# Kernel optimization log

Measured on AMD Instinct MI355X. Metric: run time of the kernel, lower is better.

The kernel has to match this reference:

```python
import jax, jax.numpy as jnp
import numpy as np
from jax import lax

# ---- config (matches init_kwargs) ----
B, T, H = 4, 2048, 1024
HU = 4 * H                 # h_up = hidden*4
LAYERS, INDEX = 12, 0
K_CLAMP, K_EPS = 60.0, 1e-8
LN_EPS = 1e-5


def setup_inputs() -> dict:
    key = jax.random.key(0)
    ks = jax.random.split(key, 9)
    s = 0.02  # weight scale
    tr01 = INDEX / (LAYERS - 1)          # time_ratio_0_to_1
    tr1pz = 1.0 - INDEX / LAYERS         # time_ratio_1_to_pz
    i_h = np.arange(H, dtype=np.float64) / H
    i_hu = np.arange(HU, dtype=np.float64)
    # per-channel decay speed / first (sized to the WKV channel dim h_up)
    decay_speed = -5.0 + 8.0 * (i_hu / (HU - 1)) ** (0.7 + 1.3 * tr01)
    zigzag = ((np.arange(HU) + 1) % 3 - 1) * 0.5
    time_first = np.log(0.3) + zigzag
    f32 = lambda a: jnp.asarray(a, jnp.float32)
    return {
        "x": jax.random.normal(ks[0], (B, T, H), jnp.float32),
        "ln0_g": jnp.ones((H,), jnp.float32), "ln0_b": jnp.zeros((H,), jnp.float32),
        "pre_g": jnp.ones((H,), jnp.float32), "pre_b": jnp.zeros((H,), jnp.float32),
        "post_g": jnp.ones((H,), jnp.float32), "post_b": jnp.zeros((H,), jnp.float32),
        "tm_decay": f32(decay_speed),
        "tm_first": f32(time_first),
        "tm_mix_k": f32(i_h ** tr1pz),
        "tm_mix_v": f32(i_h ** tr1pz + 0.3 * tr01),
        "tm_mix_r": f32(i_h ** (0.5 * tr1pz)),
        "tm_Wk": jax.random.normal(ks[1], (H, HU), jnp.float32) * s,
        "tm_Wv": jax.random.normal(ks[2], (H, HU), jnp.float32) * s,
        "tm_Wr": jax.random.normal(ks[3], (H, HU), jnp.float32) * s,
        "tm_Wo": jax.random.normal(ks[4], (HU, H), jnp.float32) * s,
        "cm_mix_k": f32(i_h ** tr1pz),
        "cm_mix_r": f32(i_h ** tr1pz),
        "cm_Wk": jax.random.normal(ks[5], (H, HU), jnp.float32) * s,
        "cm_Wv": jax.random.normal(ks[6], (HU, H), jnp.float32) * s,
        "cm_Wr": jax.random.normal(ks[7], (H, H), jnp.float32) * s,
    }


def _ln(x, g, b):
    m = jnp.mean(x, -1, keepdims=True)
    v = jnp.mean((x - m) ** 2, -1, keepdims=True)
    return (x - m) / jnp.sqrt(v + LN_EPS) * g + b


def _shift(x):  # ZeroPad2d((0,0,1,-1)): xx[:, t] = x[:, t-1], xx[:, 0] = 0
    return jnp.pad(x[:, :-1], ((0, 0), (1, 0), (0, 0)))


def _wkv(k, kv, decay, first):
    # k, kv: [B, T, HU]; decay, first: [HU]
    # wkv[t] = first*kv[t] + sum_{d>=1} decay^(d-1) * kv[t-d]  (same for k)
    def step(carry, inp):
        sk, skv = carry
        kt, kvt = inp
        out = (first * kt + sk, first * kvt + skv)
        return (kt + decay * sk, kvt + decay * skv), out
    b = k.shape[0]
    init = (jnp.zeros((b, k.shape[2]), k.dtype), jnp.zeros((b, k.shape[2]), k.dtype))
    _, (wk, wkv) = lax.scan(step, init, (jnp.swapaxes(k, 0, 1), jnp.swapaxes(kv, 0, 1)))
    return jnp.swapaxes(wk, 0, 1), jnp.swapaxes(wkv, 0, 1)


def reference(x, ln0_g, ln0_b, pre_g, pre_b, post_g, post_b,
              tm_decay, tm_first, tm_mix_k, tm_mix_v, tm_mix_r,
              tm_Wk, tm_Wv, tm_Wr, tm_Wo,
              cm_mix_k, cm_mix_r, cm_Wk, cm_Wv, cm_Wr):
    if INDEX == 0:
        x = _ln(x, ln0_g, ln0_b)

    # ---- RWKV_TM (time mix / WKV) ----
    xn = _ln(x, pre_g, pre_b)
    xx = _shift(xn)
    xk = xn * tm_mix_k + xx * (1.0 - tm_mix_k)
    xv = xn * tm_mix_v + xx * (1.0 - tm_mix_v)
    xr = xn * tm_mix_r + xx * (1.0 - tm_mix_r)
    k = jnp.exp(jnp.minimum(xk @ tm_Wk, K_CLAMP))   # [B,T,HU]
    v = xv @ tm_Wv                                  # [B,T,HU]
    r = xr @ tm_Wr                                  # [B,T,HU]
    kv = k * v
    decay = jnp.exp(-jnp.exp(tm_decay))  # per-step multiplier exp(-exp(time_decay))
    first = jnp.exp(tm_first)
    wk, wkv = _wkv(k, kv, decay, first)
    rwkv = jax.nn.sigmoid(r) * (wkv / (wk + K_EPS))
    x = x + rwkv @ tm_Wo

    # ---- RWKV_CM (channel mix) ----
    xn = _ln(x, post_g, post_b)
    xx = _shift(xn)
    xk = xn * cm_mix_k + xx * (1.0 - cm_mix_k)
    xr = xn * cm_mix_r + xx * (1.0 - cm_mix_r)
    kv = jax.nn.silu(xk @ cm_Wk) @ cm_Wv            # [B,T,H]
    x = x + (jax.nn.sigmoid(xr @ cm_Wr) + kv)
    return x
```

## Files before the change

### kernel.cpp

```cpp
#include <hip/hip_runtime.h>

#define Hdim  1024
#define Tdim  2048
#define Bdim  4
#define HUdim 4096
#define Mrows (Bdim*Tdim)
#define CHUNK 2048
#define NCH   (HUdim/CHUNK)
#define NSEG  16
#define SEGL  (Tdim/NSEG)
#define SCHUNK 16

typedef __bf16 bf16;
typedef __bf16 bf16x2 __attribute__((ext_vector_type(2)));
typedef __bf16 bf16x8 __attribute__((ext_vector_type(8)));
typedef float  floatx4 __attribute__((ext_vector_type(4)));

__device__ __forceinline__ bf16 f2bf(float x) { return (bf16)x; }

__global__ __launch_bounds__(256) void wconv_all(
    const float* __restrict__ s0, const float* __restrict__ s1, const float* __restrict__ s2,
    const float* __restrict__ s3, const float* __restrict__ s4, const float* __restrict__ s5,
    const float* __restrict__ s6,
    bf16* d0, bf16* d1, bf16* d2, bf16* d3, bf16* d4, bf16* d5, bf16* d6) {
  __shared__ float tile[64][65];
  int bid = blockIdx.x;
  const float* src; bf16* dst; int K, N, local;
  if (bid < 1024)      { src = s0; dst = d0; K = Hdim;  N = HUdim; local = bid; }
  else if (bid < 2048) { src = s1; dst = d1; K = Hdim;  N = HUdim; local = bid - 1024; }
  else if (bid < 3072) { src = s2; dst = d2; K = Hdim;  N = HUdim; local = bid - 2048; }
  else if (bid < 4096) { src = s3; dst = d3; K = HUdim; N = Hdim;  local = bid - 3072; }
  else if (bid < 5120) { src = s4; dst = d4; K = Hdim;  N = HUdim; local = bid - 4096; }
  else if (bid < 6144) { src = s5; dst = d5; K = HUdim; N = Hdim;  local = bid - 5120; }
  else                 { src = s6; dst = d6; K = Hdim;  N = Hdim;  local = bid - 6144; }
  const int nt = N >> 6;
  const int n0 = (local % nt) * 64, k0 = (local / nt) * 64;
  const int tr = threadIdx.x >> 6;
  const int tc = threadIdx.x & 63;
#pragma unroll
  for (int j = 0; j < 16; j++) {
    int r = j * 4 + tr;
    tile[r][tc] = src[(size_t)(k0 + r) * N + n0 + tc];
  }
  __syncthreads();
#pragma unroll
  for (int j = 0; j < 16; j++) {
    int r = j * 4 + tr;
    dst[(size_t)(n0 + r) * K + k0 + tc] = f2bf(tile[tc][r]);
  }
}

__device__ __forceinline__ void block_reduce4(float v[4], float* sm) {
#pragma unroll
  for (int off = 32; off > 0; off >>= 1) {
#pragma unroll
    for (int i = 0; i < 4; i++) v[i] += __shfl_down(v[i], off, 64);
  }
  const int w = threadIdx.x >> 6;
  if ((threadIdx.x & 63) == 0) {
#pragma unroll
    for (int i = 0; i < 4; i++) sm[w * 4 + i] = v[i];
  }
  __syncthreads();
#pragma unroll
  for (int i = 0; i < 4; i++) v[i] = sm[i] + sm[4 + i] + sm[8 + i] + sm[12 + i];
  __syncthreads();
}

__global__ __launch_bounds__(256) void ln_mix_tm(
    const float* __restrict__ x,
    const float* __restrict__ g0, const float* __restrict__ b0,
    const float* __restrict__ g1, const float* __restrict__ b1,
    const float* __restrict__ mk, const float* __restrict__ mv, const float* __restrict__ mr,
    float* __restrict__ x0, bf16* __restrict__ xk, bf16* __restrict__ xv, bf16* __restrict__ xr) {
  __shared__ float sm[16];
  const int bid = blockIdx.x;
  const int t = bid & (Tdim - 1);
  const int tid = threadIdx.x;
  const bool havep = (t > 0);
  const float hp = havep ? 1.f : 0.f;
  const float* rowc = x + (size_t)bid * Hdim;
  const float* rowp = havep ? (rowc - Hdim) : rowc;

  float c[4], p[4];
#pragma unroll
  for (int j = 0; j < 4; j++) c[j] = rowc[tid * 4 + j];
#pragma unroll
  for (int j = 0; j < 4; j++) p[j] = rowp[tid * 4 + j] * hp;

  float red[4] = {0.f, 0.f, 0.f, 0.f};
#pragma unroll
  for (int j = 0; j < 4; j++) { red[0] += c[j]; red[1] += c[j]*c[j]; red[2] += p[j]; red[3] += p[j]*p[j]; }
  block_reduce4(red, sm);
  const float inv = 1.f / Hdim;
  float mc = red[0]*inv, vc = red[1]*inv - mc*mc;
  float mp = red[2]*inv, vp = red[3]*inv - mp*mp;
  float sc = rsqrtf(vc + 1e-5f), sp = rsqrtf(vp + 1e-5f);

  float yc[4], yp[4];
#pragma unroll
  for (int j = 0; j < 4; j++) {
    int i = tid * 4 + j;
    yc[j] = (c[j] - mc) * sc * g0[i] + b0[i];
    yp[j] = ((p[j] - mp) * sp * g0[i] + b0[i]) * hp;
    x0[(size_t)bid * Hdim + i] = yc[j];
  }

  float r2[4] = {0.f, 0.f, 0.f, 0.f};
#pragma unroll
  for (int j = 0; j < 4; j++) { r2[0] += yc[j]; r2[1] += yc[j]*yc[j]; r2[2] += yp[j]; r2[3] += yp[j]*yp[j]; }
  block_reduce4(r2, sm);
  float mc2 = r2[0]*inv, vc2 = r2[1]*inv - mc2*mc2;
  float mp2 = r2[2]*inv, vp2 = r2[3]*inv - mp2*mp2;
  float sc2 = rsqrtf(vc2 + 1e-5f), sp2 = rsqrtf(vp2 + 1e-5f);

#pragma unroll
  for (int j = 0; j < 4; j++) {
    int i = tid * 4 + j;
    float xnc = (yc[j] - mc2) * sc2 * g1[i] + b1[i];
    float xnp = ((yp[j] - mp2) * sp2 * g1[i] + b1[i]) * hp;
    size_t o = (size_t)bid * Hdim + i;
    float a;
    a = mk[i]; xk[o] = f2bf(xnc * a + xnp * (1.f - a));
    a = mv[i]; xv[o] = f2bf(xnc * a + xnp * (1.f - a));
    a = mr[i]; xr[o] = f2bf(xnc * a + xnp * (1.f - a));
  }
}

__global__ __launch_bounds__(256) void ln_mix_cm(
    const float* __restrict__ xin,
    const float* __restrict__ g, const float* __restrict__ bb,
    const float* __restrict__ mk, const float* __restrict__ mr,
    bf16* __restrict__ xk, bf16* __restrict__ xr) {
  __shared__ float sm[16];
  const int bid = blockIdx.x;
  const int t = bid & (Tdim - 1);
  const int tid = threadIdx.x;
  const bool havep = (t > 0);
  const float hp = havep ? 1.f : 0.f;
  const float* rowc = xin + (size_t)bid * Hdim;
  const float* rowp = havep ? (rowc - Hdim) : rowc;

  float c[4], p[4];
#pragma unroll
  for (int j = 0; j < 4; j++) c[j] = rowc[tid * 4 + j];
#pragma unroll
  for (int j = 0; j < 4; j++) p[j] = rowp[tid * 4 + j] * hp;

  float red[4] = {0.f, 0.f, 0.f, 0.f};
#pragma unroll
  for (int j = 0; j < 4; j++) { red[0] += c[j]; red[1] += c[j]*c[j]; red[2] += p[j]; red[3] += p[j]*p[j]; }
  block_reduce4(red, sm);
  const float inv = 1.f / Hdim;
  float mc = red[0]*inv, vc = red[1]*inv - mc*mc;
  float mp = red[2]*inv, vp = red[3]*inv - mp*mp;
  float sc = rsqrtf(vc + 1e-5f), sp = rsqrtf(vp + 1e-5f);

#pragma unroll
  for (int j = 0; j < 4; j++) {
    int i = tid * 4 + j;
    float xnc = (c[j] - mc) * sc * g[i] + bb[i];
    float xnp = ((p[j] - mp) * sp * g[i] + bb[i]) * hp;
    size_t o = (size_t)bid * Hdim + i;
    float a;
    a = mk[i]; xk[o] = f2bf(xnc * a + xnp * (1.f - a));
    a = mr[i]; xr[o] = f2bf(xnc * a + xnp * (1.f - a));
  }
}

__global__ __launch_bounds__(64) void wkv_part(
    const bf16* __restrict__ Kb, const bf16* __restrict__ Vb,
    float* __restrict__ stK, float* __restrict__ stKV,
    const float* __restrict__ tdec) {
  const int seg = blockIdx.x & (NSEG - 1);
  const int rest = blockIdx.x >> 4;
  const int b = rest >> 4, g = rest & 15;
  const int c = (g << 7) + (threadIdx.x << 1);
  const float d0 = __expf(-__expf(tdec[c]));
  const float d1 = __expf(-__expf(tdec[c + 1]));
  size_t base = ((size_t)b * Tdim + (size_t)seg * SEGL) * CHUNK + c;
  float sk0 = 0.f, skv0 = 0.f, sk1 = 0.f, skv1 = 0.f;
  for (int t0 = 0; t0 < SEGL; t0 += SCHUNK) {
    bf16x2 kk[SCHUNK], vv[SCHUNK];
#pragma unroll
    for (int j = 0; j < SCHUNK; j++) {
      size_t idx = base + (size_t)(t0 + j) * CHUNK;
      kk[j] = *(const bf16x2*)(Kb + idx);
      vv[j] = *(const bf16x2*)(Vb + idx);
    }
#pragma unroll
    for (int j = 0; j < SCHUNK; j++) {
      float k0 = (float)kk[j][0], k1 = (float)kk[j][1];
      float v0 = (float)vv[j][0], v1 = (float)vv[j][1];
      sk0  = fmaf(d0, sk0, k0);   skv0 = fmaf(d0, skv0, k0 * v0);
      sk1  = fmaf(d1, sk1, k1);   skv1 = fmaf(d1, skv1, k1 * v1);
    }
  }
  size_t so = ((size_t)seg * Bdim + b) * CHUNK + c;
  stK[so]      = sk0;  stK[so + 1]  = sk1;
  stKV[so]     = skv0; stKV[so + 1] = skv1;
}

__global__ __launch_bounds__(64) void wkv_emit(
    const bf16* __restrict__ Kb, const bf16* __restrict__ Vb,
    const bf16* SRb, bf16* Pb,
    const float* __restrict__ stK, const float* __restrict__ stKV,
    const float* __restrict__ tdec, const float* __restrict__ tfst) {
  const int seg = blockIdx.x & (NSEG - 1);
  const int rest = blockIdx.x >> 4;
  const int b = rest >> 4, g = rest & 15;
  const int c = (g << 7) + (threadIdx.x << 1);
  const float ed0 = __expf(tdec[c]),     ed1 = __expf(tdec[c + 1]);
  const float d0  = __expf(-ed0),        d1  = __expf(-ed1);
  const float df0 = __expf(-ed0 * (float)SEGL);
  const float df1 = __expf(-ed1 * (float)SEGL);
  const float f0  = __expf(tfst[c]),     f1  = __expf(tfst[c + 1]);

  float sk0 = 0.f, skv0 = 0.f, sk1 = 0.f, skv1 = 0.f;
  for (int j = 0; j < seg; j++) {
    size_t so = ((size_t)j * Bdim + b) * CHUNK + c;
    sk0  = fmaf(df0, sk0,  stK[so]);      sk1  = fmaf(df1, sk1,  stK[so + 1]);
    skv0 = fmaf(df0, skv0, stKV[so]);     skv1 = fmaf(df1, skv1, stKV[so + 1]);
  }

  size_t base = ((size_t)b * Tdim + (size_t)seg * SEGL) * CHUNK + c;
  for (int t0 = 0; t0 < SEGL; t0 += SCHUNK) {
    bf16x2 kk[SCHUNK], vv[SCHUNK], rr[SCHUNK];
#pragma unroll
    for (int j = 0; j < SCHUNK; j++) {
      size_t idx = base + (size_t)(t0 + j) * CHUNK;
      kk[j] = *(const bf16x2*)(Kb + idx);
      vv[j] = *(const bf16x2*)(Vb + idx);
      rr[j] = *(const bf16x2*)(SRb + idx);
    }
#pragma unroll
    for (int j = 0; j < SCHUNK; j++) {
      size_t idx = base + (size_t)(t0 + j) * CHUNK;
      float k0 = (float)kk[j][0], k1 = (float)kk[j][1];
      float v0 = (float)vv[j][0], v1 = (float)vv[j][1];
      float kv0 = k0 * v0, kv1 = k1 * v1;
      float wk0  = fmaf(f0, k0, sk0) + 1e-8f;
      float wk1  = fmaf(f1, k1, sk1) + 1e-8f;
      float wkv0 = fmaf(f0, kv0, skv0);
      float wkv1 = fmaf(f1, kv1, skv1);
      bf16x2 out;
      out[0] = f2bf((float)rr[j][0] * wkv0 * __builtin_amdgcn_rcpf(wk0));
      out[1] = f2bf((float)rr[j][1] * wkv1 * __builtin_amdgcn_rcpf(wk1));
      *(bf16x2*)(Pb + idx) = out;
      sk0  = fmaf(d0, sk0, k0);   skv0 = fmaf(d0, skv0, kv0);
      sk1  = fmaf(d1, sk1, k1);   skv1 = fmaf(d1, skv1, kv1);
    }
  }
}

__device__ __forceinline__ void gld_lds(const bf16* g, bf16* l) {
  __builtin_amdgcn_global_load_lds(
      (const __attribute__((address_space(1))) void*)(g),
      (__attribute__((address_space(3))) void*)(l),
      16, 0, 0);
}

__device__ __forceinline__ void swz(int s, int gm, int& m_t, int& n_t) {
  const int mpx  = gm >> 3;
  const int xcd  = s & 7;
  const int ss   = s >> 3;
  const int pass = mpx << 1;
  const int ng   = ss / pass;
  const int rem  = ss - ng * pass;
  m_t = xcd * mpx + (rem >> 1);
  n_t = (ng << 1) + (rem & 1);
}

__device__ __forceinline__ void mm_core64(
    const bf16* A, const bf16* Bt, int lda, int ldb, int K,
    long m0, long n0, int wv, int lane, int wm, int wn,
    bf16* As, bf16* Bs, floatx4 acc[4][4]) {
  const int srow = wv * 32 + (lane >> 2);
  const int scol = (((lane & 3) - ((lane >> 3) & 3)) & 3) * 8;
  const bf16* gA = A + (m0 + srow) * (long)lda + scol;
  const bf16* gB = Bt + (n0 + srow) * (long)ldb + scol;
  const long skipA = 16L * lda;
  const long skipB = 16L * ldb;
  bf16* lA = As + wv * 1024;
  bf16* lB = Bs + wv * 1024;
  const int pg = ((lane >> 4) + ((lane >> 1) & 3)) & 3;
  const bf16* fa = As + ((wm * 64) + (lane & 15)) * 32 + pg * 8;
  const bf16* fb = Bs + ((wn * 64) + (lane & 15)) * 32 + pg * 8;

  const int ksteps = K >> 6;
  for (int kt = 0; kt < ksteps; ++kt) {
    __syncthreads();
    gld_lds(gA, lA);             gld_lds(gA + skipA, lA + 512);
    gld_lds(gA + 32, lA + 4096); gld_lds(gA + 32 + skipA, lA + 4096 + 512);
    gld_lds(gB, lB);             gld_lds(gB + skipB, lB + 512);
    gld_lds(gB + 32, lB + 4096); gld_lds(gB + 32 + skipB, lB + 4096 + 512);
    gA += 64; gB += 64;
    __syncthreads();
#pragma unroll
    for (int s = 0; s < 2; s++) {
      bf16x8 af[4], bfr[4];
#pragma unroll
      for (int i = 0; i < 4; i++) {
        af[i]  = *(const bf16x8*)(fa + s * 4096 + i * 512);
        bfr[i] = *(const bf16x8*)(fb + s * 4096 + i * 512);
      }
#pragma unroll
      for (int mt = 0; mt < 4; mt++)
#pragma unroll
        for (int nt = 0; nt < 4; nt++)
          acc[mt][nt] = __builtin_amdgcn_mfma_f32_16x16x32_bf16(af[mt], bfr[nt], acc[mt][nt], 0, 0, 0);
    }
  }
}

enum { E_EXP = 0, E_BF16 = 1, E_SIG = 2, E_ADD1 = 3, E_SILU = 4, E_F32 = 5, E_SIGADD2 = 6 };

template <int EPI>
__device__ __forceinline__ void epilogue(
    floatx4 acc[4][4], void* Cout, const void* aux1, const void* aux2,
    long m0, long n0, int ldc, int lane, int wm, int wn) {
  const int r0 = wm * 64 + ((lane >> 4) << 2);
  const int c0 = wn * 64 + (lane & 15);
#pragma unroll
  for (int mt = 0; mt < 4; mt++) {
#pragma unroll
    for (int i = 0; i < 4; i++) {
      long r = m0 + r0 + mt * 16 + i;
      long bidx = r * (long)ldc + n0 + c0;
#pragma unroll
      for (int nt = 0; nt < 4; nt++) {
        long idx = bidx + nt * 16;
        float v = acc[mt][nt][i];
        if constexpr (EPI == E_EXP) {
          ((bf16*)Cout)[idx] = f2bf(__expf(fminf(v, 60.f)));
        } else if constexpr (EPI == E_BF16) {
          ((bf16*)Cout)[idx] = f2bf(v);
        } else if constexpr (EPI == E_SIG) {
          ((bf16*)Cout)[idx] = f2bf(1.f / (1.f + __expf(-v)));
        } else if constexpr (EPI == E_ADD1) {
          float prev = ((const float*)aux1)[idx];
          ((float*)Cout)[idx] = v + prev;
        } else if constexpr (EPI == E_SILU) {
          ((bf16*)Cout)[idx] = f2bf(v / (1.f + __expf(-v)));
        } else if constexpr (EPI == E_F32) {
          ((float*)Cout)[idx] = v;
        } else {
          float a1 = ((const float*)aux1)[idx];
          float a2 = ((const float*)aux2)[idx];
          ((float*)Cout)[idx] = a1 + 1.f / (1.f + __expf(-v)) + a2;
        }
      }
    }
  }
}

template <int EPI, int MT>
__global__ __launch_bounds__(256) void gemm_bt(
    const bf16* __restrict__ A, const bf16* __restrict__ Bt,
    void* Cout, const void* aux1, const void* aux2,
    int lda, int ldb, int ldc, int K, int gm, int gn) {
  __shared__ __align__(16) bf16 As[2 * 128 * 32];
  __shared__ __align__(16) bf16 Bs[2 * 128 * 32];
  const int tid = threadIdx.x;
  const int lane = tid & 63;
  const int wv = tid >> 6;
  const int wm = wv >> 1, wn = wv & 1;
  int m_t, n_t;
  swz(blockIdx.x, gm, m_t, n_t);
  const long n0 = (long)n_t * 128;

#pragma unroll
  for (int sm = 0; sm < MT; sm++) {
    const long m0 = (long)m_t * (128 * MT) + sm * 128;
    floatx4 acc[4][4];
#pragma unroll
    for (int i = 0; i < 4; i++)
#pragma unroll
      for (int j = 0; j < 4; j++) acc[i][j] = (floatx4){0.f, 0.f, 0.f, 0.f};
    mm_core64(A, Bt, lda, ldb, K, m0, n0, wv, lane, wm, wn, As, Bs, acc);
    epilogue<EPI>(acc, Cout, aux1, aux2, m0, n0, ldc, lane, wm, wn);
  }
}

__device__ __forceinline__ void mm_core256(
    const bf16* __restrict__ A, const bf16* __restrict__ Bt,
    int lda, int ldb, int K, long m0, long n0,
    int wv, int lane, bf16* Lds, floatx4 acc[8][4]) {
  const int wm = wv >> 2, wn = wv & 3;
  const int rA0 = wm * 128 + (wv & 3) * 16;
  const int rB0 = (wv >> 1) * 64 + (wv & 1) * 16;
  const int rl  = lane >> 2;
  const int scol = (((lane & 3) - ((lane >> 3) & 3)) & 3) * 8;
  const bf16* gA = A + (m0 + rA0 + rl) * (long)lda + scol;
  const bf16* gB = Bt + (n0 + rB0 + rl) * (long)ldb + scol;
  bf16* lA = Lds + rA0 * 32;
  bf16* lB = Lds + 16384 + rB0 * 32;

  const int pg = ((lane >> 4) + ((lane >> 1) & 3)) & 3;
  const bf16* fa0 = Lds + (wm * 128 + (lane & 15)) * 32 + pg * 8;
  const bf16* fb0 = Lds + 16384 + (wn * 64 + (lane & 15)) * 32 + pg * 8;

#define STGA8(buf, h, kt) do { \
    const bf16* _s = gA + (long)(h) * 64 * lda + (kt) * 64; \
    bf16* _d = lA + (buf) * 32768 + (h) * 2048; \
    gld_lds(_s, _d); gld_lds(_s + 32, _d + 8192); } while (0)
#define STGB8(buf, h, kt) do { \
    const bf16* _s = gB + (long)(h) * 32 * ldb + (kt) * 64; \
    bf16* _d = lB + (buf) * 32768 + (h) * 1024; \
    gld_lds(_s, _d); gld_lds(_s + 32, _d + 8192); } while (0)

  STGA8(0, 0, 0); STGA8(0, 1, 0); STGB8(0, 0, 0); STGB8(0, 1, 0);
  STGA8(1, 0, 1); STGB8(1, 0, 1);
  asm volatile("s_waitcnt vmcnt(4)" ::: "memory");
  __builtin_amdgcn_s_barrier();

  const int niter = K >> 7;
  for (int it = 0; it < niter; ++it) {
    const int kt0 = it << 1;
    const bool notlast = (it != niter - 1);
#pragma unroll
    for (int ph = 0; ph < 8; ++ph) {
      const int buf = ph >> 2;
      const int mq = (ph >> 1) & 1, nq = ph & 1;
      bf16x8 a[4][2], b[2][2];
      const bf16* fa = fa0 + buf * 32768 + mq * 2048;
      const bf16* fb = fb0 + buf * 32768 + nq * 1024;
#pragma unroll
      for (int mf = 0; mf < 4; ++mf) {
        a[mf][0] = *(const bf16x8*)(fa + mf * 512);
        a[mf][1] = *(const bf16x8*)(fa + mf * 512 + 8192);
      }
#pragma unroll
      for (int nf = 0; nf < 2; ++nf) {
        b[nf][0] = *(const bf16x8*)(fb + nf * 512);
        b[nf][1] = *(const bf16x8*)(fb + nf * 512 + 8192);
      }
      __builtin_amdgcn_sched_barrier(0);
      if (ph == 0)      STGA8(1, 1, kt0 + 1);
      else if (ph == 1) STGB8(1, 1, kt0 + 1);
      else if (notlast) {
        if (ph == 2)      STGA8(0, 0, kt0 + 2);
        else if (ph == 3) STGB8(0, 0, kt0 + 2);
        else if (ph == 4) STGA8(0, 1, kt0 + 2);
        else if (ph == 5) STGB8(0, 1, kt0 + 2);
        else if (ph == 6) STGA8(1, 0, kt0 + 3);
        else              STGB8(1, 0, kt0 + 3);
      }
      if (ph == 3) {
        if (notlast) { asm volatile("s_waitcnt vmcnt(4)" ::: "memory"); }
        else         { asm volatile("s_waitcnt vmcnt(0)" ::: "memory"); }
      } else if (ph == 7 && notlast) {
        asm volatile("s_waitcnt vmcnt(4)" ::: "memory");
      }
      __builtin_amdgcn_s_barrier();
      asm volatile("s_waitcnt lgkmcnt(0)" ::: "memory");
      __builtin_amdgcn_s_setprio(1);
#pragma unroll
      for (int mf = 0; mf < 4; ++mf)
#pragma unroll
        for (int nf = 0; nf < 2; ++nf) {
          acc[mq*4+mf][nq*2+nf] = __builtin_amdgcn_mfma_f32_16x16x32_bf16(
              a[mf][0], b[nf][0], acc[mq*4+mf][nq*2+nf], 0, 0, 0);
          acc[mq*4+mf][nq*2+nf] = __builtin_amdgcn_mfma_f32_16x16x32_bf16(
              a[mf][1], b[nf][1], acc[mq*4+mf][nq*2+nf], 0, 0, 0);
        }
      __builtin_amdgcn_s_setprio(0);
      __builtin_amdgcn_s_barrier();
    }
  }
#undef STGA8
#undef STGB8
}

template <int EPI>
__global__ __launch_bounds__(512, 2) void gemm8(
    const bf16* __restrict__ A, const bf16* __restrict__ Bt,
    void* Cout, const void* aux1, const void* aux2,
    int lda, int ldb, int ldc, int K, int gm, int gn) {
  __shared__ __align__(16) bf16 Lds[65536];
  const int tid = threadIdx.x;
  const int lane = tid & 63;
  const int wv = tid >> 6;
  int m_t, n_t;
  swz(blockIdx.x, gm, m_t, n_t);
  const long m0 = (long)m_t * 256, n0 = (long)n_t * 256;
  floatx4 acc[8][4];
#pragma unroll
  for (int i = 0; i < 8; i++)
#pragma unroll
    for (int j = 0; j < 4; j++) acc[i][j] = (floatx4){0.f, 0.f, 0.f, 0.f};
  mm_core256(A, Bt, lda, ldb, K, m0, n0, wv, lane, Lds, acc);

  const int wm = wv >> 2, wn = wv & 3;
  const int r0 = wm * 128 + ((lane >> 4) << 2);
  const int c0 = wn * 64 + (lane & 15);
#pragma unroll
  for (int mf = 0; mf < 8; ++mf) {
#pragma unroll
    for (int i = 0; i < 4; ++i) {
      long r = m0 + r0 + mf * 16 + i;
      long bidx = r * (long)ldc + n0 + c0;
#pragma unroll
      for (int nf = 0; nf < 4; ++nf) {
        long idx = bidx + nf * 16;
        float v = acc[mf][nf][i];
        if constexpr (EPI == E_SILU) {
          ((bf16*)Cout)[idx] = f2bf(v / (1.f + __expf(-v)));
        } else if constexpr (EPI == E_BF16) {
          ((bf16*)Cout)[idx] = f2bf(v);
        } else if constexpr (EPI == E_F32) {
          ((float*)Cout)[idx] = v;
        } else if constexpr (EPI == E_ADD1) {
          float prev = ((const float*)aux1)[idx];
          ((float*)Cout)[idx] = v + prev;
        }
      }
    }
  }
}

__global__ __launch_bounds__(512, 2) void proj8(
    const bf16* __restrict__ xk, const bf16* __restrict__ xv, const bf16* __restrict__ xr,
    const bf16* __restrict__ Wk, const bf16* __restrict__ Wv, const bf16* __restrict__ Wr,
    bf16* Kc, bf16* Vc, bf16* SRc, int gm, int gn) {
  __shared__ __align__(16) bf16 Lds[65536];
  const int per = gm * gn;
  const int sub = blockIdx.x / per;
  const int s   = blockIdx.x - sub * per;
  const int tid = threadIdx.x;
  const int lane = tid & 63;
  const int wv = tid >> 6;
  int m_t, n_t;
  swz(s, gm, m_t, n_t);
  const long m0 = (long)m_t * 256, n0 = (long)n_t * 256;

  const bf16* A  = (sub == 0) ? xk : (sub == 1) ? xv : xr;
  const bf16* Bt = (sub == 0) ? Wk : (sub == 1) ? Wv : Wr;
  bf16*       C  = (sub == 0) ? Kc : (sub == 1) ? Vc : SRc;

  floatx4 acc[8][4];
#pragma unroll
  for (int i = 0; i < 8; i++)
#pragma unroll
    for (int j = 0; j < 4; j++) acc[i][j] = (floatx4){0.f, 0.f, 0.f, 0.f};
  mm_core256(A, Bt, Hdim, Hdim, Hdim, m0, n0, wv, lane, Lds, acc);

  const int wm = wv >> 2, wn = wv & 3;
  const int r0 = wm * 128 + ((lane >> 4) << 2);
  const int c0 = wn * 64 + (lane & 15);
#pragma unroll
  for (int mf = 0; mf < 8; ++mf) {
#pragma unroll
    for (int i = 0; i < 4; ++i) {
      long r = m0 + r0 + mf * 16 + i;
      long bidx = r * (long)CHUNK + n0 + c0;
#pragma unroll
      for (int nf = 0; nf < 4; ++nf) {
        long idx = bidx + nf * 16;
        float v = acc[mf][nf][i];
        float o;
        if (sub == 0)      o = __expf(fminf(v, 60.f));
        else if (sub == 1) o = v;
        else               o = 1.f / (1.f + __expf(-v));
        C[idx] = f2bf(o);
      }
    }
  }
}

extern "C" void kernel_launch(void* const* d_in, const int* in_sizes, int n_in,
                              void* d_out, int out_size, void* d_ws, size_t ws_size,
                              hipStream_t stream) {
  (void)in_sizes; (void)n_in; (void)out_size; (void)ws_size;
  const float* x        = (const float*)d_in[0];
  const float* ln0_g    = (const float*)d_in[1];
  const float* ln0_b    = (const float*)d_in[2];
  const float* pre_g    = (const float*)d_in[3];
  const float* pre_b    = (const float*)d_in[4];
  const float* post_g   = (const float*)d_in[5];
  const float* post_b   = (const float*)d_in[6];
  const float* tm_decay = (const float*)d_in[7];
  const float* tm_first = (const float*)d_in[8];
  const float* tm_mix_k = (const float*)d_in[9];
  const float* tm_mix_v = (const float*)d_in[10];
  const float* tm_mix_r = (const float*)d_in[11];
  const float* tm_Wk    = (const float*)d_in[12];
  const float* tm_Wv    = (const float*)d_in[13];
  const float* tm_Wr    = (const float*)d_in[14];
  const float* tm_Wo    = (const float*)d_in[15];
  const float* cm_mix_k = (const float*)d_in[16];
  const float* cm_mix_r = (const float*)d_in[17];
  const float* cm_Wk    = (const float*)d_in[18];
  const float* cm_Wv    = (const float*)d_in[19];
  const float* cm_Wr    = (const float*)d_in[20];

  char* ws = (char*)d_ws;
  bf16*  WkT  = (bf16*)(ws + 0);
  bf16*  WvT  = (bf16*)(ws + 8388608);
  bf16*  WrT  = (bf16*)(ws + 16777216);
  bf16*  WoT  = (bf16*)(ws + 25165824);
  bf16*  cWkT = (bf16*)(ws + 33554432);
  bf16*  cWvT = (bf16*)(ws + 41943040);
  bf16*  cWrT = (bf16*)(ws + 50331648);
  float* xres = (float*)(ws + 52428800);
  bf16*  xk   = (bf16*)(ws + 85983232);
  bf16*  xv   = (bf16*)(ws + 102760448);
  bf16*  xr   = (bf16*)(ws + 119537664);
  bf16*  Kc   = (bf16*)(ws + 136314880);
  bf16*  Vc   = (bf16*)(ws + 169869312);
  bf16*  SRc  = (bf16*)(ws + 203423744);
  float* stK  = (float*)(ws + 236978176);
  float* stKV = (float*)(ws + 237502464);
  bf16*  xk2  = (bf16*)(ws + 136314880);
  bf16*  xr2  = (bf16*)(ws + 153092096);
  bf16*  hbuf = (bf16*)(ws + 169869312);
  float* hv   = (float*)(ws + 85983232);

  dim3 blk(256);
  wconv_all<<<6400, blk, 0, stream>>>(tm_Wk, tm_Wv, tm_Wr, tm_Wo, cm_Wk, cm_Wv, cm_Wr,
                                      WkT, WvT, WrT, WoT, cWkT, cWvT, cWrT);

  ln_mix_tm<<<Mrows, blk, 0, stream>>>(x, ln0_g, ln0_b, pre_g, pre_b,
                                       tm_mix_k, tm_mix_v, tm_mix_r, xres, xk, xv, xr);

  const int scan_grid = NSEG * Bdim * (CHUNK / 128);
  const int GM = Mrows / 128;
  const int GM8 = Mrows / 256;
  const int GN8p = CHUNK / 256;
  for (int ch = 0; ch < NCH; ch++) {
    const long woff = (long)ch * CHUNK;
    proj8<<<3 * GM8 * GN8p, dim3(512), 0, stream>>>(
        xk, xv, xr, WkT + woff * Hdim, WvT + woff * Hdim, WrT + woff * Hdim,
        Kc, Vc, SRc, GM8, GN8p);

    wkv_part<<<scan_grid, dim3(64), 0, stream>>>(
        Kc, Vc, stK, stKV, tm_decay + woff);
    wkv_emit<<<scan_grid, dim3(64), 0, stream>>>(
        Kc, Vc, SRc, SRc, stK, stKV, tm_decay + woff, tm_first + woff);

    gemm_bt<E_ADD1, 1><<<GM * (Hdim/128), blk, 0, stream>>>(
        SRc, WoT + woff, xres, xres, nullptr, CHUNK, HUdim, Hdim, CHUNK, GM, Hdim/128);
  }

  ln_mix_cm<<<Mrows, blk, 0, stream>>>(xres, post_g, post_b, cm_mix_k, cm_mix_r, xk2, xr2);

  gemm8<E_SILU><<<GM8 * (HUdim/256), dim3(512), 0, stream>>>(
      xk2, cWkT, hbuf, nullptr, nullptr, Hdim, Hdim, HUdim, Hdim, GM8, HUdim/256);

  gemm_bt<E_F32, 1><<<GM * (Hdim/128), blk, 0, stream>>>(
      hbuf, cWvT, hv, nullptr, nullptr, HUdim, HUdim, Hdim, CHUNK, GM, Hdim/128);
  gemm_bt<E_ADD1, 1><<<GM * (Hdim/128), blk, 0, stream>>>(
      hbuf + CHUNK, cWvT + CHUNK, hv, hv, nullptr, HUdim, HUdim, Hdim, CHUNK, GM, Hdim/128);

  gemm_bt<E_SIGADD2, 1><<<GM * (Hdim/128), blk, 0, stream>>>(
      xr2, cWrT, (float*)d_out, xres, hv, Hdim, Hdim, Hdim, Hdim, GM, Hdim/128);
}
```

Measured before the change: 926.5 us.

## Reuse LDS fragments across phases with snake order and deeper prefetch

The GEMM inner loop now visits the four sub-tile quadrants of each buffer in a snake order (00,01,11,10). A and B register fragments stay live across phases, so each quadrant loads only the operand that changed instead of reloading both from LDS. The global-to-LDS staging schedule is reordered to keep more loads in flight, with vmcnt thresholds adjusted to match, and the barrier before the last quadrant is dropped. This cuts LDS read traffic and barrier count at the cost of extra registers and a more fragile wait-count schedule that could race if the counts are wrong.

```diff
diff --git a/kernel.cpp b/kernel.cpp
--- a/kernel.cpp
+++ b/kernel.cpp
@@ -409,60 +409,82 @@
     bf16* _d = lB + (buf) * 32768 + (h) * 1024; \
     gld_lds(_s, _d); gld_lds(_s + 32, _d + 8192); } while (0)
 
-  STGA8(0, 0, 0); STGA8(0, 1, 0); STGB8(0, 0, 0); STGB8(0, 1, 0);
-  STGA8(1, 0, 1); STGB8(1, 0, 1);
-  asm volatile("s_waitcnt vmcnt(4)" ::: "memory");
+  STGA8(0, 0, 0); STGB8(0, 0, 0); STGB8(0, 1, 0); STGA8(0, 1, 0);
+  STGA8(1, 0, 1); STGB8(1, 0, 1); STGB8(1, 1, 1);
+  asm volatile("s_waitcnt vmcnt(10)" ::: "memory");
   __builtin_amdgcn_s_barrier();
 
   const int niter = K >> 7;
+  bf16x8 a[4][2];
+  bf16x8 b[2][2][2];
   for (int it = 0; it < niter; ++it) {
     const int kt0 = it << 1;
     const bool notlast = (it != niter - 1);
 #pragma unroll
     for (int ph = 0; ph < 8; ++ph) {
+      const int q   = ph & 3;
       const int buf = ph >> 2;
-      const int mq = (ph >> 1) & 1, nq = ph & 1;
-      bf16x8 a[4][2], b[2][2];
+      const int mq  = q >> 1;
+      const int nq  = (q >> 1) ^ (q & 1);
       const bf16* fa = fa0 + buf * 32768 + mq * 2048;
       const bf16* fb = fb0 + buf * 32768 + nq * 1024;
-#pragma unroll
-      for (int mf = 0; mf < 4; ++mf) {
-        a[mf][0] = *(const bf16x8*)(fa + mf * 512);
-        a[mf][1] = *(const bf16x8*)(fa + mf * 512 + 8192);
-      }
-#pragma unroll
-      for (int nf = 0; nf < 2; ++nf) {
-        b[nf][0] = *(const bf16x8*)(fb + nf * 512);
-        b[nf][1] = *(const bf16x8*)(fb + nf * 512 + 8192);
+      if (q == 0) {
+#pragma unroll
+        for (int mf = 0; mf < 4; ++mf) {
+          a[mf][0] = *(const bf16x8*)(fa + mf * 512);
+          a[mf][1] = *(const bf16x8*)(fa + mf * 512 + 8192);
+        }
+#pragma unroll
+        for (int nf = 0; nf < 2; ++nf) {
+          b[0][nf][0] = *(const bf16x8*)(fb + nf * 512);
+          b[0][nf][1] = *(const bf16x8*)(fb + nf * 512 + 8192);
+        }
+      } else if (q == 1) {
+#pragma unroll
+        for (int nf = 0; nf < 2; ++nf) {
+          b[1][nf][0] = *(const bf16x8*)(fb + nf * 512);
+          b[1][nf][1] = *(const bf16x8*)(fb + nf * 512 + 8192);
+        }
+      } else if (q == 2) {
+#pragma unroll
+        for (int mf = 0; mf < 4; ++mf) {
+          a[mf][0] = *(const bf16x8*)(fa + mf * 512);
+          a[mf][1] = *(const bf16x8*)(fa + mf * 512 + 8192);
+        }
       }
       __builtin_amdgcn_sched_barrier(0);
-      if (ph == 0)      STGA8(1, 1, kt0 + 1);
-      else if (ph == 1) STGB8(1, 1, kt0 + 1);
+      if (ph == 0)            STGA8(1, 1, kt0 + 1);
       else if (notlast) {
-        if (ph == 2)      STGA8(0, 0, kt0 + 2);
-        else if (ph == 3) STGB8(0, 0, kt0 + 2);
+        if (ph == 1)      STGA8(0, 0, kt0 + 2);
+        else if (ph == 2) STGB8(0, 0, kt0 + 2);
+        else if (ph == 3) STGB8(0, 1, kt0 + 2);
         else if (ph == 4) STGA8(0, 1, kt0 + 2);
-        else if (ph == 5) STGB8(0, 1, kt0 + 2);
-        else if (ph == 6) STGA8(1, 0, kt0 + 3);
-        else              STGB8(1, 0, kt0 + 3);
-      }
-      if (ph == 3) {
-        if (notlast) { asm volatile("s_waitcnt vmcnt(4)" ::: "memory"); }
-        else         { asm volatile("s_waitcnt vmcnt(0)" ::: "memory"); }
-      } else if (ph == 7 && notlast) {
-        asm volatile("s_waitcnt vmcnt(4)" ::: "memory");
-      }
-      __builtin_amdgcn_s_barrier();
-      asm volatile("s_waitcnt lgkmcnt(0)" ::: "memory");
+        else if (ph == 5) STGA8(1, 0, kt0 + 3);
+        else if (ph == 6) STGB8(1, 0, kt0 + 3);
+        else              STGB8(1, 1, kt0 + 3);
+      }
+      if (notlast) {
+        if (ph == 0 || ph == 1 || ph == 4 || ph == 5)
+          asm volatile("s_waitcnt vmcnt(10)" ::: "memory");
+        else if (ph == 3 || ph == 7)
+          asm volatile("s_waitcnt vmcnt(12)" ::: "memory");
+      } else {
+        if (ph == 0)      asm volatile("s_waitcnt vmcnt(10)" ::: "memory");
+        else if (ph == 1) asm volatile("s_waitcnt vmcnt(0)" ::: "memory");
+      }
+      if (q != 3) {
+        __builtin_amdgcn_s_barrier();
+        asm volatile("s_waitcnt lgkmcnt(0)" ::: "memory");
+      }
       __builtin_amdgcn_s_setprio(1);
 #pragma unroll
       for (int mf = 0; mf < 4; ++mf)
 #pragma unroll
         for (int nf = 0; nf < 2; ++nf) {
           acc[mq*4+mf][nq*2+nf] = __builtin_amdgcn_mfma_f32_16x16x32_bf16(
-              a[mf][0], b[nf][0], acc[mq*4+mf][nq*2+nf], 0, 0, 0);
+              a[mf][0], b[nq][nf][0], acc[mq*4+mf][nq*2+nf], 0, 0, 0);
           acc[mq*4+mf][nq*2+nf] = __builtin_amdgcn_mfma_f32_16x16x32_bf16(
-              a[mf][1], b[nf][1], acc[mq*4+mf][nq*2+nf], 0, 0, 0);
+              a[mf][1], b[nq][nf][1], acc[mq*4+mf][nq*2+nf], 0, 0, 0);
         }
       __builtin_amdgcn_s_setprio(0);
       __builtin_amdgcn_s_barrier();
```

Result: slower. 959.6 us (+3.6%).
